# Kernel optimization log

Measured on AMD Instinct MI355X. Metric: run time of the kernel, lower is better.

Reference implementation:

```python
import jax, jax.numpy as jnp
import numpy as np

B, NV, NQ, D, H = 8, 1024, 512, 1024, 8
HEAD_DIM = D // H


def _linear(x, W, b):
    # torch nn.Linear: x @ W.T + b, W: [out, in]
    return x @ W.T + b


def setup_inputs() -> dict:
    key = jax.random.key(0)
    ks = jax.random.split(key, 10)
    s = 0.02
    f32 = jnp.float32
    return {
        "v": jax.random.normal(ks[0], (B, NV, D), f32),
        "q": jax.random.normal(ks[1], (B, NQ, D), f32),
        "Wg_v4q": jax.random.normal(ks[2], (D, D), f32) * s,
        "bg_v4q": jnp.zeros((D,), f32),
        "Wg_q4v": jax.random.normal(ks[3], (D, D), f32) * s,
        "bg_q4v": jnp.zeros((D,), f32),
        "Wv": jax.random.normal(ks[4], (3 * D, D), f32) * s,
        "bv": jnp.zeros((3 * D,), f32),
        "Wq": jax.random.normal(ks[5], (3 * D, D), f32) * s,
        "bq": jnp.zeros((3 * D,), f32),
        "Wvo": jax.random.normal(ks[6], (D, D), f32) * s,
        "bvo": jnp.zeros((D,), f32),
        "Wqo": jax.random.normal(ks[7], (D, D), f32) * s,
        "bqo": jnp.zeros((D,), f32),
    }


def _mha(qh, kh, vh):
    # qh/kh/vh: [B, N, D] -> head-batched attention, faithful to per-head loop + concat
    b, n, _ = qh.shape
    m = kh.shape[1]
    qh = qh.reshape(b, n, H, HEAD_DIM)
    kh = kh.reshape(b, m, H, HEAD_DIM)
    vh = vh.reshape(b, m, H, HEAD_DIM)
    scores = jnp.einsum("bnhd,bmhd->bhnm", qh, kh) / jnp.sqrt(jnp.float32(HEAD_DIM))
    attn = jax.nn.softmax(scores, axis=-1)
    out = jnp.einsum("bhnm,bmhd->bnhd", attn, vh)
    return out.reshape(b, n, D)


def reference(v, q, Wg_v4q, bg_v4q, Wg_q4v, bg_q4v, Wv, bv, Wq, bq, Wvo, bvo, Wqo, bqo):
    # DyIntraModalityUpdate.forward (drop=0.0)
    v_mean = v.mean(axis=1)
    q_mean = q.mean(axis=1)
    v4q_gate = jax.nn.sigmoid(_linear(jax.nn.relu(v_mean), Wg_v4q, bg_v4q))[:, None, :]
    q4v_gate = jax.nn.sigmoid(_linear(jax.nn.relu(q_mean), Wg_q4v, bg_q4v))[:, None, :]
    v_trans = _linear(jax.nn.relu(v), Wv, bv)
    q_trans = _linear(jax.nn.relu(q), Wq, bq)
    v_k, v_q, v_v = jnp.split(v_trans, 3, axis=2)
    q_k, q_q, q_v = jnp.split(q_trans, 3, axis=2)
    new_vq = (1.0 + q4v_gate) * v_q
    new_vk = (1.0 + q4v_gate) * v_k
    new_qq = (1.0 + v4q_gate) * q_q
    new_qk = (1.0 + v4q_gate) * q_k
    v_update = _mha(new_vq, new_vk, v_v)
    q_update = _mha(new_qq, new_qk, q_v)
    updated_v = _linear(v + v_update, Wvo, bvo)
    updated_q = _linear(q + q_update, Wqo, bqo)
    return (updated_v, updated_q)
```

## Files before the change

kernel.cpp:

```cpp
#include <hip/hip_runtime.h>

typedef unsigned short u16;
typedef unsigned int u32;
typedef __attribute__((ext_vector_type(8))) short short8;
typedef __attribute__((ext_vector_type(4))) float floatx4;

__device__ __forceinline__ float bf2f(u16 x) {
    union { u32 u; float f; } c; c.u = ((u32)x) << 16; return c.f;
}
__device__ __forceinline__ u16 f2bf(float f) {
    union { float f; u32 u; } c; c.f = f;
    return (u16)((c.u + 0x7FFFu + ((c.u >> 16) & 1u)) >> 16);
}
__device__ __forceinline__ u32 pack_bf16(float lo, float hi) {
    return ((u32)f2bf(lo)) | (((u32)f2bf(hi)) << 16);
}

#define GLD_LDS(g, l) __builtin_amdgcn_global_load_lds( \
    (const __attribute__((address_space(1))) u32*)(g),  \
    (__attribute__((address_space(3))) u32*)(l), 16, 0, 0)


__global__ __launch_bounds__(256) void prep_kernel(
    const float* __restrict__ v, const float* __restrict__ q,
    u16* __restrict__ crv, u16* __restrict__ crq, float* __restrict__ pmean,
    const float* __restrict__ Wq, const float* __restrict__ Wqo,
    const float* __restrict__ Wv, const float* __restrict__ Wvo,
    u16* __restrict__ cWtQ, u16* __restrict__ cWoQ,
    u16* __restrict__ cWtV, u16* __restrict__ cWoV)
{
    const int bid = blockIdx.x;
    if (bid < 4096) {
        int i = bid * 256 + threadIdx.x;
        const float* src; u16* dst; int ii;
        if (i < 393216)      { src = Wq;  dst = cWtQ; ii = i; }
        else if (i < 524288) { src = Wqo; dst = cWoQ; ii = i - 393216; }
        else if (i < 917504) { src = Wv;  dst = cWtV; ii = i - 524288; }
        else                 { src = Wvo; dst = cWoV; ii = i - 917504; }
        float4 a = ((const float4*)src)[2 * ii];
        float4 b = ((const float4*)src)[2 * ii + 1];
        float vv[8] = {a.x, a.y, a.z, a.w, b.x, b.y, b.z, b.w};
        short8 o;
#pragma unroll
        for (int j = 0; j < 8; j++) o[j] = (short)f2bf(vv[j]);
        ((short8*)dst)[ii] = o;
        return;
    }
    const int lbid = bid - 4096;
    const int idx = (lbid & 63) * 256 + threadIdx.x;
    const int j = lbid >> 6;
    const int half = idx >> 13;
    const int lidx = idx & 8191;
    const int b = lidx >> 10, d = lidx & 1023;
    float s = 0.f;
    if (half == 0) {
        const float* p = v + (size_t)b * 1024 * 1024 + (size_t)(j * 128) * 1024 + d;
        u16* cw = crv + (size_t)b * 1024 * 1024 + (size_t)(j * 128) * 1024 + d;
        for (int n = 0; n < 128; n++) {
            float x = p[(size_t)n * 1024];
            cw[(size_t)n * 1024] = f2bf(fmaxf(x, 0.f));
            s += x;
        }
    } else {
        const float* p = q + (size_t)b * 512 * 1024 + (size_t)(j * 64) * 1024 + d;
        u16* cw = crq + (size_t)b * 512 * 1024 + (size_t)(j * 64) * 1024 + d;
        for (int n = 0; n < 64; n++) {
            float x = p[(size_t)n * 1024];
            cw[(size_t)n * 1024] = f2bf(fmaxf(x, 0.f));
            s += x;
        }
    }
    pmean[j * 16384 + idx] = s;
}


__global__ __launch_bounds__(256) void gate_kernel(
    const float* __restrict__ pmean,
    const float* __restrict__ Wg0, const float* __restrict__ bg0, float* __restrict__ g0,
    const float* __restrict__ Wg1, const float* __restrict__ bg1, float* __restrict__ g1)
{
    int gw = blockIdx.x * 4 + (threadIdx.x >> 6);
    int lane = threadIdx.x & 63;
    const int half = gw >> 13;
    const int lw = gw & 8191;
    const int b = lw >> 10, n = lw & 1023;
    const float* wr = (half ? Wg1 : Wg0) + (size_t)n * 1024;
    const float invN = half ? (1.f / 512.f) : (1.f / 1024.f);
    const int pbase = half * 8192 + b * 1024;
    float acc = 0.f;
    for (int k = lane; k < 1024; k += 64) {
        float m = 0.f;
#pragma unroll
        for (int j = 0; j < 8; j++) m += pmean[j * 16384 + pbase + k];
        acc += fmaxf(m * invN, 0.f) * wr[k];
    }
#pragma unroll
    for (int msk = 1; msk < 64; msk <<= 1) acc += __shfl_xor(acc, msk, 64);
    if (lane == 0) {
        float xg = acc + (half ? bg1 : bg0)[n];
        (half ? g1 : g0)[lw] = 1.f + 1.f / (1.f + __expf(-xg));
    }
}


__global__ __launch_bounds__(256) void gemm_bt_kernel(
    const u16* __restrict__ A, const u16* __restrict__ W,
    const float* __restrict__ bias, const float* __restrict__ gate,
    u16* __restrict__ Ch, float* __restrict__ Cf,
    int M, int N, int K, int seq, int gateN)
{
    __shared__ u16 As[2][128 * 32];
    __shared__ u16 Bs[2][128 * 32];

    const int tid = threadIdx.x;
    const int wave = tid >> 6, lane = tid & 63, quad = lane >> 4, l15 = lane & 15;

    const u32 gx = gridDim.x;
    const u32 flat = blockIdx.y * gx + blockIdx.x;
    const u32 per = (gx * gridDim.y) >> 3;
    const u32 swz = (flat & 7) * per + (flat >> 3);
    const int m0 = (int)(swz / gx) * 128, n0 = (int)(swz % gx) * 128;

    const int wm = (wave >> 1) * 64, wn = (wave & 1) * 64;

    floatx4 acc[4][4] = {};

    const int e0 = (wave * 1024 + lane * 16) >> 1;
    const int sr0 = e0 >> 5, sc0 = e0 & 31;
    const int e1 = e0 + 2048;
    const int sr1 = e1 >> 5, sc1 = e1 & 31;
    const size_t aoff0 = (size_t)(m0 + sr0) * K + sc0;
    const size_t aoff1 = (size_t)(m0 + sr1) * K + sc1;
    const size_t boff0 = (size_t)(n0 + sr0) * K + sc0;
    const size_t boff1 = (size_t)(n0 + sr1) * K + sc1;

    GLD_LDS(A + aoff0, As[0] + wave * 512);
    GLD_LDS(A + aoff1, As[0] + 2048 + wave * 512);
    GLD_LDS(W + boff0, Bs[0] + wave * 512);
    GLD_LDS(W + boff1, Bs[0] + 2048 + wave * 512);
    __syncthreads();

    int cur = 0;
    for (int k0 = 0; k0 < K; k0 += 32) {
        const int nxt = cur ^ 1;
        if (k0 + 32 < K) {
            GLD_LDS(A + aoff0 + k0 + 32, As[nxt] + wave * 512);
            GLD_LDS(A + aoff1 + k0 + 32, As[nxt] + 2048 + wave * 512);
            GLD_LDS(W + boff0 + k0 + 32, Bs[nxt] + wave * 512);
            GLD_LDS(W + boff1 + k0 + 32, Bs[nxt] + 2048 + wave * 512);
        }

        short8 af[4], bfr[4];
#pragma unroll
        for (int i = 0; i < 4; i++) {
            af[i]  = *(const short8*)(As[cur] + (wm + i * 16 + l15) * 32 + quad * 8);
            bfr[i] = *(const short8*)(Bs[cur] + (wn + i * 16 + l15) * 32 + quad * 8);
        }
#pragma unroll
        for (int mi = 0; mi < 4; mi++)
#pragma unroll
            for (int ni = 0; ni < 4; ni++)
                acc[mi][ni] = __builtin_amdgcn_mfma_f32_16x16x32_bf16(af[mi], bfr[ni], acc[mi][ni], 0, 0, 0);
        __syncthreads();
        cur = nxt;
    }

    const int b = m0 / seq;
#pragma unroll
    for (int ni = 0; ni < 4; ni++) {
        const int ncol = n0 + wn + ni * 16 + l15;
        const float bsv = bias[ncol];
        float g = 1.f;
        if (gate != nullptr && ncol < gateN) g = gate[b * 1024 + (ncol & 1023)];
#pragma unroll
        for (int mi = 0; mi < 4; mi++) {
            const int row = m0 + wm + mi * 16 + quad * 4;
#pragma unroll
            for (int r = 0; r < 4; r++) {
                float val = (acc[mi][ni][r] + bsv) * g;
                size_t idx = (size_t)(row + r) * N + ncol;
                if (Cf) Cf[idx] = val; else Ch[idx] = f2bf(val);
            }
        }
    }
}


__global__ __launch_bounds__(512, 2) void attn_kernel(
    const u16* __restrict__ T, const float* __restrict__ X,
    u16* __restrict__ U, int N)
{
    __shared__ __align__(16) u16 Ks[2][64 * 128];
    __shared__ __align__(16) u16 Vs[2][128 * 64];

    const int tid = threadIdx.x;
    const int wave = tid >> 6, lane = tid & 63, quad = (lane >> 4) & 3, l15 = lane & 15;

    const int f = blockIdx.y * gridDim.x + blockIdx.x;
    const int i3 = f >> 3;
    const int qb = i3 % gridDim.x;
    const int bh = (f & 7) * 8 + i3 / gridDim.x;
    const int b = bh >> 3, h = bh & 7;

    const size_t base = (size_t)b * N * 3072;
    const int kcol = h * 128, qcol = 1024 + h * 128, vcol = 2048 + h * 128;

    short8 qf[4];
    const int qrow0 = qb * 128 + wave * 16;
#pragma unroll
    for (int c = 0; c < 4; c++)
        qf[c] = *(const short8*)(T + base + (size_t)(qrow0 + l15) * 3072
                                   + qcol + c * 32 + quad * 8);

    floatx4 o[8] = {};
    float mrow = -1e30f, lrow = 0.f;
    const float scale = 0.08838834764831845f;

    int kst_kv[2], kst_d[2];
#pragma unroll
    for (int r = 0; r < 2; r++) {
        int ob = r * 8192 + wave * 1024 + lane * 16;
        int kv = ob >> 8;
        kst_kv[r] = kv;
        kst_d[r] = ((((ob >> 4) & 15) ^ (kv & 15)) << 3);
    }
    const int vkv = (tid & 31) * 2;
    const int vd8 = tid >> 5;

    short8 v0, v1;
#pragma unroll
    for (int r = 0; r < 2; r++)
        GLD_LDS(T + base + (size_t)kst_kv[r] * 3072 + kcol + kst_d[r],
                Ks[0] + r * 4096 + wave * 512);
    {
        const u16* vp = T + base + (size_t)vkv * 3072 + vcol + vd8 * 8;
        v0 = *(const short8*)vp;
        v1 = *(const short8*)(vp + 3072);
    }
#pragma unroll
    for (int j = 0; j < 8; j++) {
        u32 wv = ((u32)(u16)v0[j]) | (((u32)(u16)v1[j]) << 16);
        *(u32*)((char*)Vs[0] + (size_t)(vd8 * 8 + j) * 128
                + ((((vkv >> 3) ^ j)) << 4) + ((vkv * 2) & 15)) = wv;
    }
    __syncthreads();

    int cur = 0;
    for (int kt = 0; kt < N; kt += 64) {
        const int nxt = cur ^ 1;
        const bool more = (kt + 64) < N;

        if (more) {
#pragma unroll
            for (int r = 0; r < 2; r++)
                GLD_LDS(T + base + (size_t)(kt + 64 + kst_kv[r]) * 3072 + kcol + kst_d[r],
                        Ks[nxt] + r * 4096 + wave * 512);
            const u16* vp = T + base + (size_t)(kt + 64 + vkv) * 3072 + vcol + vd8 * 8;
            v0 = *(const short8*)vp;
            v1 = *(const short8*)(vp + 3072);
        }

        float p[4][4];
        __builtin_amdgcn_s_setprio(1);
#pragma unroll
        for (int ni = 0; ni < 4; ni++) {
            short8 kf[4];
#pragma unroll
            for (int c = 0; c < 4; c++)
                kf[c] = *(const short8*)(Ks[cur] + (ni * 16 + l15) * 128
                                            + (((c * 4 + quad) ^ l15) << 3));
            floatx4 s = {0.f, 0.f, 0.f, 0.f};
#pragma unroll
            for (int c = 0; c < 4; c++)
                s = __builtin_amdgcn_mfma_f32_16x16x32_bf16(kf[c], qf[c], s, 0, 0, 0);
#pragma unroll
            for (int r = 0; r < 4; r++) p[ni][r] = s[r] * scale;
        }
        __builtin_amdgcn_s_setprio(0);

        {
            float tm = p[0][0];
#pragma unroll
            for (int ni = 0; ni < 4; ni++)
#pragma unroll
                for (int r = 0; r < 4; r++) tm = fmaxf(tm, p[ni][r]);
            tm = fmaxf(tm, __shfl_xor(tm, 16, 64));
            tm = fmaxf(tm, __shfl_xor(tm, 32, 64));
            const bool need = __any(tm > mrow + 8.f);
            if (need) {
                float mnew = fmaxf(mrow, tm);
                float alpha = __expf(mrow - mnew);
                mrow = mnew;
                float ps = 0.f;
#pragma unroll
                for (int ni = 0; ni < 4; ni++)
#pragma unroll
                    for (int r = 0; r < 4; r++) {
                        float pe = __expf(p[ni][r] - mnew);
                        p[ni][r] = pe;
                        ps += pe;
                    }
                ps += __shfl_xor(ps, 16, 64);
                ps += __shfl_xor(ps, 32, 64);
                lrow = lrow * alpha + ps;
#pragma unroll
                for (int r = 0; r < 4; r++) {
                    float ab = __shfl(alpha, quad * 4 + r, 64);
#pragma unroll
                    for (int nt = 0; nt < 8; nt++) o[nt][r] *= ab;
                }
            } else {
                float ps = 0.f;
#pragma unroll
                for (int ni = 0; ni < 4; ni++)
#pragma unroll
                    for (int r = 0; r < 4; r++) {
                        float pe = __expf(p[ni][r] - mrow);
                        p[ni][r] = pe;
                        ps += pe;
                    }
                ps += __shfl_xor(ps, 16, 64);
                ps += __shfl_xor(ps, 32, 64);
                lrow += ps;
            }
        }

        u32* pw = (u32*)((char*)Vs[nxt] + wave * 2048);
        const int xs = (l15 & 7) << 2;
#pragma unroll
        for (int ni = 0; ni < 4; ni++)
#pragma unroll
            for (int s2 = 0; s2 < 2; s2++)
                pw[l15 * 32 + ((ni * 8 + quad * 2 + s2) ^ xs)]
                    = pack_bf16(p[ni][2 * s2], p[ni][2 * s2 + 1]);
        short8 pf[2];
#pragma unroll
        for (int kc = 0; kc < 2; kc++)
            pf[kc] = *(const short8*)(pw + l15 * 32 + ((kc * 16 + quad * 4) ^ xs));

        __builtin_amdgcn_s_setprio(1);
#pragma unroll
        for (int nt = 0; nt < 8; nt++) {
#pragma unroll
            for (int kc = 0; kc < 2; kc++) {
                short8 vf = *(const short8*)(Vs[cur] + (nt * 16 + l15) * 64
                                + (((kc * 4 + quad) ^ (l15 & 7)) << 3));
                o[nt] = __builtin_amdgcn_mfma_f32_16x16x32_bf16(pf[kc], vf, o[nt], 0, 0, 0);
            }
        }
        __builtin_amdgcn_s_setprio(0);

        if (more) {
#pragma unroll
            for (int j = 0; j < 8; j++) {
                u32 wv = ((u32)(u16)v0[j]) | (((u32)(u16)v1[j]) << 16);
                *(u32*)((char*)Vs[nxt] + (size_t)(vd8 * 8 + j) * 128
                        + ((((vkv >> 3) ^ j)) << 4) + ((vkv * 2) & 15)) = wv;
            }
        }
        __syncthreads();
        cur = nxt;
    }

    const size_t ub = (size_t)b * N * 1024;
#pragma unroll
    for (int r = 0; r < 4; r++) {
        float lb = __shfl(lrow, quad * 4 + r, 64);
        float inv = 1.f / lb;
        const size_t row = qb * 128 + wave * 16 + quad * 4 + r;
#pragma unroll
        for (int nt = 0; nt < 8; nt++) {
            const size_t idx = ub + row * 1024 + h * 128 + nt * 16 + l15;
            U[idx] = f2bf(X[idx] + o[nt][r] * inv);
        }
    }
}


extern "C" void kernel_launch(void* const* d_in, const int* in_sizes, int n_in,
                              void* d_out, int out_size, void* d_ws, size_t ws_size,
                              hipStream_t stream) {
    (void)in_sizes; (void)n_in; (void)out_size; (void)ws_size;
    const float* v   = (const float*)d_in[0];
    const float* q   = (const float*)d_in[1];
    const float* Wg_v4q = (const float*)d_in[2];
    const float* bg_v4q = (const float*)d_in[3];
    const float* Wg_q4v = (const float*)d_in[4];
    const float* bg_q4v = (const float*)d_in[5];
    const float* Wv  = (const float*)d_in[6];
    const float* bv  = (const float*)d_in[7];
    const float* Wq  = (const float*)d_in[8];
    const float* bq  = (const float*)d_in[9];
    const float* Wvo = (const float*)d_in[10];
    const float* bvo = (const float*)d_in[11];
    const float* Wqo = (const float*)d_in[12];
    const float* bqo = (const float*)d_in[13];
    float* out = (float*)d_out;

    char* w = (char*)d_ws;
    float* pmean = (float*)(w + 0);
    float* gv4q  = (float*)(w + 524288);
    float* gq4v  = (float*)(w + 557056);
    u16* crv  = (u16*)(w + 1048576);
    u16* cWtV = (u16*)(w + 17825792);
    u16* cWoV = (u16*)(w + 24117248);
    u16* cWtQ = (u16*)(w + 26214400);
    u16* cWoQ = (u16*)(w + 32505856);
    u16* crq  = (u16*)(w + 34603008);
    u16* vt   = (u16*)(w + 26214400);

    u16* qt   = (u16*)out;
    u16* qres = crq;
    u16* vres = crv;

    prep_kernel<<<4608, 256, 0, stream>>>(v, q, crv, crq, pmean,
                                          Wq, Wqo, Wv, Wvo,
                                          cWtQ, cWoQ, cWtV, cWoV);
    gate_kernel<<<4096, 256, 0, stream>>>(pmean, Wg_v4q, bg_v4q, gv4q,
                                          Wg_q4v, bg_q4v, gq4v);

    gemm_bt_kernel<<<dim3(24, 32), 256, 0, stream>>>(crq, cWtQ, bq, gv4q, qt, nullptr,
                                                     4096, 3072, 1024, 512, 2048);
    attn_kernel<<<dim3(4, 64), 512, 0, stream>>>(qt, q, qres, 512);
    gemm_bt_kernel<<<dim3(8, 32), 256, 0, stream>>>(qres, cWoQ, bqo, nullptr, nullptr,
                                                    out + 8388608, 4096, 1024, 1024, 512, 0);

    gemm_bt_kernel<<<dim3(24, 64), 256, 0, stream>>>(crv, cWtV, bv, gq4v, vt, nullptr,
                                                     8192, 3072, 1024, 1024, 2048);
    attn_kernel<<<dim3(8, 64), 512, 0, stream>>>(vt, v, vres, 1024);
    gemm_bt_kernel<<<dim3(8, 64), 256, 0, stream>>>(vres, cWoV, bvo, nullptr, nullptr,
                                                    out, 8192, 1024, 1024, 1024, 0);
}
```

Measured before the change: 461.4 us.

## Replace 128x128 GEMM with 256x256-tile 8-wave kernel using split-phase pipelined loads

Replaces the 128x128, 4-wave bf16 GEMM with a 256x256-tile, 8-wave kernel where each wave computes 128x64. The K loop processes 64 per iteration in two 32-wide halves and interleaves A and B staging loads with the MFMA phases. It uses explicit vmcnt waits, s_barrier and s_setprio to overlap global-to-LDS copies with compute. This raises data reuse per loaded byte and hides load latency, but needs 128KB of LDS (one block per CU) and makes the grids much smaller (e.g. 64 blocks for the Q output projection), which risks underfilling the GPU.

Result: slower. 524.2 us (+13.6%).

```diff
diff --git a/kernel.cpp b/kernel.cpp
--- a/kernel.cpp
+++ b/kernel.cpp
@@ -103,67 +103,133 @@
 }
 
 
-__global__ __launch_bounds__(256) void gemm_bt_kernel(
+__global__ __launch_bounds__(512, 1) void gemm256_kernel(
     const u16* __restrict__ A, const u16* __restrict__ W,
     const float* __restrict__ bias, const float* __restrict__ gate,
     u16* __restrict__ Ch, float* __restrict__ Cf,
     int M, int N, int K, int seq, int gateN)
 {
-    __shared__ u16 As[2][128 * 32];
-    __shared__ u16 Bs[2][128 * 32];
+    __shared__ __align__(16) u16 As[2][2][8192];
+    __shared__ __align__(16) u16 Bs[2][2][8192];
 
     const int tid = threadIdx.x;
-    const int wave = tid >> 6, lane = tid & 63, quad = lane >> 4, l15 = lane & 15;
+    const int wave = tid >> 6, lane = tid & 63, quad = (lane >> 4) & 3, l15 = lane & 15;
 
     const u32 gx = gridDim.x;
     const u32 flat = blockIdx.y * gx + blockIdx.x;
     const u32 per = (gx * gridDim.y) >> 3;
     const u32 swz = (flat & 7) * per + (flat >> 3);
-    const int m0 = (int)(swz / gx) * 128, n0 = (int)(swz % gx) * 128;
-
-    const int wm = (wave >> 1) * 64, wn = (wave & 1) * 64;
-
-    floatx4 acc[4][4] = {};
-
-    const int e0 = (wave * 1024 + lane * 16) >> 1;
-    const int sr0 = e0 >> 5, sc0 = e0 & 31;
-    const int e1 = e0 + 2048;
-    const int sr1 = e1 >> 5, sc1 = e1 & 31;
-    const size_t aoff0 = (size_t)(m0 + sr0) * K + sc0;
-    const size_t aoff1 = (size_t)(m0 + sr1) * K + sc1;
-    const size_t boff0 = (size_t)(n0 + sr0) * K + sc0;
-    const size_t boff1 = (size_t)(n0 + sr1) * K + sc1;
-
-    GLD_LDS(A + aoff0, As[0] + wave * 512);
-    GLD_LDS(A + aoff1, As[0] + 2048 + wave * 512);
-    GLD_LDS(W + boff0, Bs[0] + wave * 512);
-    GLD_LDS(W + boff1, Bs[0] + 2048 + wave * 512);
-    __syncthreads();
-
+    const int m0 = (int)(swz / gx) * 256, n0 = (int)(swz % gx) * 256;
+
+    const int wm = (wave >> 2) * 128, wn = (wave & 3) * 64;
+
+    floatx4 acc[8][4] = {};
+
+    const int srow = wave * 16 + (lane >> 2);
+    const int scol = (lane & 3) * 8;
+    const size_t aoff0 = (size_t)(m0 + srow) * K + scol;
+    const size_t aoff1 = aoff0 + (size_t)128 * K;
+    const size_t boff0 = (size_t)(n0 + srow) * K + scol;
+    const size_t boff1 = boff0 + (size_t)128 * K;
+
+#define STAGE_A(buf, h, kof) do { \
+    GLD_LDS(A + aoff0 + (kof), &As[buf][h][wave * 512]); \
+    GLD_LDS(A + aoff1 + (kof), &As[buf][h][4096 + wave * 512]); } while (0)
+#define STAGE_B(buf, h, kof) do { \
+    GLD_LDS(W + boff0 + (kof), &Bs[buf][h][wave * 512]); \
+    GLD_LDS(W + boff1 + (kof), &Bs[buf][h][4096 + wave * 512]); } while (0)
+
+    STAGE_A(0, 0, 0);
+    STAGE_B(0, 0, 0);
+    STAGE_A(0, 1, 32);
+    STAGE_B(0, 1, 32);
+
+    const int NT = K >> 6;
     int cur = 0;
-    for (int k0 = 0; k0 < K; k0 += 32) {
+    for (int t = 0; t < NT; t++) {
         const int nxt = cur ^ 1;
-        if (k0 + 32 < K) {
-            GLD_LDS(A + aoff0 + k0 + 32, As[nxt] + wave * 512);
-            GLD_LDS(A + aoff1 + k0 + 32, As[nxt] + 2048 + wave * 512);
-            GLD_LDS(W + boff0 + k0 + 32, Bs[nxt] + wave * 512);
-            GLD_LDS(W + boff1 + k0 + 32, Bs[nxt] + 2048 + wave * 512);
-        }
-
-        short8 af[4], bfr[4];
-#pragma unroll
-        for (int i = 0; i < 4; i++) {
-            af[i]  = *(const short8*)(As[cur] + (wm + i * 16 + l15) * 32 + quad * 8);
-            bfr[i] = *(const short8*)(Bs[cur] + (wn + i * 16 + l15) * 32 + quad * 8);
-        }
-#pragma unroll
-        for (int mi = 0; mi < 4; mi++)
+        const int kof = (t + 1) << 6;
+        const bool more = (t + 1) < NT;
+
+        short8 af[4], bf[4];
+
+        if (more) {
+            STAGE_A(nxt, 0, kof);
+            asm volatile("s_waitcnt vmcnt(6)" ::: "memory");
+        } else {
+            asm volatile("s_waitcnt vmcnt(4)" ::: "memory");
+        }
+        __builtin_amdgcn_s_barrier();
+        __builtin_amdgcn_sched_barrier(0);
+#pragma unroll
+        for (int ni = 0; ni < 4; ni++)
+            bf[ni] = *(const short8*)(&As[0][0][0] + ((size_t)&Bs[cur][0][0] - (size_t)&As[0][0][0]) / 2
+                     + (wn + ni * 16 + l15) * 32 + quad * 8);
+#pragma unroll
+        for (int i = 0; i < 4; i++)
+            af[i] = *(const short8*)(&As[cur][0][(wm + i * 16 + l15) * 32 + quad * 8]);
+        __builtin_amdgcn_s_setprio(1);
+#pragma unroll
+        for (int i = 0; i < 4; i++)
 #pragma unroll
             for (int ni = 0; ni < 4; ni++)
-                acc[mi][ni] = __builtin_amdgcn_mfma_f32_16x16x32_bf16(af[mi], bfr[ni], acc[mi][ni], 0, 0, 0);
-        __syncthreads();
+                acc[i][ni] = __builtin_amdgcn_mfma_f32_16x16x32_bf16(af[i], bf[ni], acc[i][ni], 0, 0, 0);
+        __builtin_amdgcn_s_setprio(0);
+        __builtin_amdgcn_s_barrier();
+
+        if (more) STAGE_B(nxt, 0, kof);
+#pragma unroll
+        for (int i = 0; i < 4; i++)
+            af[i] = *(const short8*)(&As[cur][0][(wm + (i + 4) * 16 + l15) * 32 + quad * 8]);
+        __builtin_amdgcn_s_setprio(1);
+#pragma unroll
+        for (int i = 0; i < 4; i++)
+#pragma unroll
+            for (int ni = 0; ni < 4; ni++)
+                acc[i + 4][ni] = __builtin_amdgcn_mfma_f32_16x16x32_bf16(af[i], bf[ni], acc[i + 4][ni], 0, 0, 0);
+        __builtin_amdgcn_s_setprio(0);
+        __builtin_amdgcn_s_barrier();
+
+        if (more) {
+            STAGE_A(nxt, 1, kof + 32);
+            asm volatile("s_waitcnt vmcnt(6)" ::: "memory");
+        } else {
+            asm volatile("s_waitcnt vmcnt(0)" ::: "memory");
+        }
+        __builtin_amdgcn_s_barrier();
+        __builtin_amdgcn_sched_barrier(0);
+#pragma unroll
+        for (int ni = 0; ni < 4; ni++)
+            bf[ni] = *(const short8*)(&Bs[cur][1][(wn + ni * 16 + l15) * 32 + quad * 8]);
+#pragma unroll
+        for (int i = 0; i < 4; i++)
+            af[i] = *(const short8*)(&As[cur][1][(wm + i * 16 + l15) * 32 + quad * 8]);
+        __builtin_amdgcn_s_setprio(1);
+#pragma unroll
+        for (int i = 0; i < 4; i++)
+#pragma unroll
+            for (int ni = 0; ni < 4; ni++)
+                acc[i][ni] = __builtin_amdgcn_mfma_f32_16x16x32_bf16(af[i], bf[ni], acc[i][ni], 0, 0, 0);
+        __builtin_amdgcn_s_setprio(0);
+        __builtin_amdgcn_s_barrier();
+
+        if (more) STAGE_B(nxt, 1, kof + 32);
+#pragma unroll
+        for (int i = 0; i < 4; i++)
+            af[i] = *(const short8*)(&As[cur][1][(wm + (i + 4) * 16 + l15) * 32 + quad * 8]);
+        __builtin_amdgcn_s_setprio(1);
+#pragma unroll
+        for (int i = 0; i < 4; i++)
+#pragma unroll
+            for (int ni = 0; ni < 4; ni++)
+                acc[i + 4][ni] = __builtin_amdgcn_mfma_f32_16x16x32_bf16(af[i], bf[ni], acc[i + 4][ni], 0, 0, 0);
+        __builtin_amdgcn_s_setprio(0);
+        __builtin_amdgcn_s_barrier();
+
         cur = nxt;
     }
+#undef STAGE_A
+#undef STAGE_B
 
     const int b = m0 / seq;
 #pragma unroll
@@ -173,7 +239,7 @@
         float g = 1.f;
         if (gate != nullptr && ncol < gateN) g = gate[b * 1024 + (ncol & 1023)];
 #pragma unroll
-        for (int mi = 0; mi < 4; mi++) {
+        for (int mi = 0; mi < 8; mi++) {
             const int row = m0 + wm + mi * 16 + quad * 4;
 #pragma unroll
             for (int r = 0; r < 4; r++) {
@@ -419,15 +485,15 @@
     gate_kernel<<<4096, 256, 0, stream>>>(pmean, Wg_v4q, bg_v4q, gv4q,
                                           Wg_q4v, bg_q4v, gq4v);
 
-    gemm_bt_kernel<<<dim3(24, 32), 256, 0, stream>>>(crq, cWtQ, bq, gv4q, qt, nullptr,
+    gemm256_kernel<<<dim3(12, 16), 512, 0, stream>>>(crq, cWtQ, bq, gv4q, qt, nullptr,
                                                      4096, 3072, 1024, 512, 2048);
     attn_kernel<<<dim3(4, 64), 512, 0, stream>>>(qt, q, qres, 512);
-    gemm_bt_kernel<<<dim3(8, 32), 256, 0, stream>>>(qres, cWoQ, bqo, nullptr, nullptr,
+    gemm256_kernel<<<dim3(4, 16), 512, 0, stream>>>(qres, cWoQ, bqo, nullptr, nullptr,
                                                     out + 8388608, 4096, 1024, 1024, 512, 0);
 
-    gemm_bt_kernel<<<dim3(24, 64), 256, 0, stream>>>(crv, cWtV, bv, gq4v, vt, nullptr,
+    gemm256_kernel<<<dim3(12, 32), 512, 0, stream>>>(crv, cWtV, bv, gq4v, vt, nullptr,
                                                      8192, 3072, 1024, 1024, 2048);
     attn_kernel<<<dim3(8, 64), 512, 0, stream>>>(vt, v, vres, 1024);
-    gemm_bt_kernel<<<dim3(8, 64), 256, 0, stream>>>(vres, cWoV, bvo, nullptr, nullptr,
+    gemm256_kernel<<<dim3(4, 32), 512, 0, stream>>>(vres, cWoV, bvo, nullptr, nullptr,
                                                     out, 8192, 1024, 1024, 1024, 0);
 }
```
